# Performance work log

Measured on AMD Instinct MI355X. Metric: run time of the kernel, lower is better.

The kernel has to match this reference:

```python
import jax, jax.numpy as jnp
import numpy as np

B = 4096
D0, D1 = 256, 64


def setup_inputs() -> dict:
    key = jax.random.key(0)
    k0, k1, k2, k3 = jax.random.split(key, 4)
    return {
        "s0": jax.random.normal(k0, (B, D0), dtype=jnp.float32),
        "s1": jax.random.normal(k1, (B, D1), dtype=jnp.float32),
        "t0": jax.random.normal(k2, (B, D0), dtype=jnp.float32),
        "t1": jax.random.normal(k3, (B, D1), dtype=jnp.float32),
    }


def _gaussian_kernel(source, target):
    # feats: [2B, D]
    feats = jnp.concatenate([source, target], axis=0)
    n = feats.shape[0]
    # pairwise squared distances [2B, 2B] via the Gram-matrix identity
    # (same math as ((x - y) ** 2).sum(-1), avoids the [N, N, D] intermediate)
    sq = jnp.sum(feats * feats, axis=-1)
    dist = sq[:, None] + sq[None, :] - 2.0 * (feats @ feats.T)
    # median-heuristic bandwidth with num_kernels=1: gamma = (n^2 - n) / sum(dist)
    gamma = (n * n - n) / jnp.sum(jax.lax.stop_gradient(dist))
    return jnp.exp(-dist * gamma)


def reference(s0, s1, t0, t1):
    # joint kernel: elementwise product of per-stream Gaussian kernels
    k = _gaussian_kernel(s0, t0) * _gaussian_kernel(s1, t1)
    b = s0.shape[0]
    s2s = k[:b, :b]
    t2t = k[b:, b:]
    s2t = k[:b, b:]
    return jnp.mean(s2s + t2t - 2.0 * s2t)
```

## Files before the change

kernel.cpp:

```cpp
#include <hip/hip_runtime.h>
#include <hip/hip_fp8.h>

#define B_ROWS 4096
#define NTOT   8192
#define D0     256
#define D1     64
#define KDIM   320
#define NSB    128
#define NTILE  64
#define NTRI   2080

typedef __attribute__((ext_vector_type(4))) float f32x4;
typedef __attribute__((ext_vector_type(2))) long long2v;

#define OFF_GAM   0
#define OFF_PQ0   32
#define OFF_PQ1   544
#define OFF_P0    1056
#define OFF_P1    132128
#define OFF_R     164896
#define OFF_BSUM  197664
#define OFF_PHI   214304

__device__ __forceinline__ void load_lds16(const void* g, void* l) {
    __builtin_amdgcn_global_load_lds(
        (const __attribute__((address_space(1))) void*)g,
        (__attribute__((address_space(3))) void*)l, 16, 0, 0);
}

#define VMCNT(n) asm volatile("s_waitcnt vmcnt(" #n ")" ::: "memory")
#define BAR()    do { asm volatile("" ::: "memory");            \
                      __builtin_amdgcn_s_barrier();             \
                      asm volatile("" ::: "memory"); } while (0)

__global__ __launch_bounds__(256) void k_stats(
    const float* __restrict__ s0, const float* __restrict__ s1,
    const float* __restrict__ t0, const float* __restrict__ t1,
    float* __restrict__ part0, float* __restrict__ part1,
    float* __restrict__ pq0, float* __restrict__ pq1) {
    __shared__ float sh0[4][256];
    __shared__ float sh1[4][64];
    __shared__ float shq[4][2];
    int t = threadIdx.x, wv = t >> 6, lane = t & 63;
    int rb = blockIdx.x * 64;
    int c4 = lane * 4;
    int rr = wv;

    f32x4 cs = {0.f, 0.f, 0.f, 0.f};
    float q0 = 0.f;
    #pragma unroll 4
    for (int k = 0; k < 16; ++k) {
        int row = rb + rr + k * 4;
        const float* b0 = (row < B_ROWS) ? s0 + (size_t)row * D0 : t0 + (size_t)(row - B_ROWS) * D0;
        f32x4 v = *(const f32x4*)(b0 + c4);
        cs.x += v.x; cs.y += v.y; cs.z += v.z; cs.w += v.w;
        q0 += v.x * v.x + v.y * v.y + v.z * v.z + v.w * v.w;
    }
    *(f32x4*)&sh0[rr][c4] = cs;

    float cs1 = 0.f, q1 = 0.f;
    #pragma unroll 4
    for (int k = 0; k < 16; ++k) {
        int row = rb + rr + k * 4;
        const float* b1 = (row < B_ROWS) ? s1 + (size_t)row * D1 : t1 + (size_t)(row - B_ROWS) * D1;
        float v = b1[lane];
        cs1 += v; q1 += v * v;
    }
    sh1[rr][lane] = cs1;

    #pragma unroll
    for (int o = 32; o; o >>= 1) { q0 += __shfl_xor(q0, o, 64); q1 += __shfl_xor(q1, o, 64); }
    if (lane == 0) { shq[wv][0] = q0; shq[wv][1] = q1; }
    __syncthreads();

    part0[blockIdx.x * D0 + t] = sh0[0][t] + sh0[1][t] + sh0[2][t] + sh0[3][t];
    if (t < D1) part1[blockIdx.x * D1 + t] = sh1[0][t] + sh1[1][t] + sh1[2][t] + sh1[3][t];
    if (t == 0) {
        pq0[blockIdx.x] = shq[0][0] + shq[1][0] + shq[2][0] + shq[3][0];
        pq1[blockIdx.x] = shq[0][1] + shq[1][1] + shq[2][1] + shq[3][1];
    }
}

__global__ __launch_bounds__(256) void k_gamma(
    const float* __restrict__ pq0, const float* __restrict__ pq1,
    const float* __restrict__ part0, const float* __restrict__ part1,
    float* __restrict__ gam) {
    __shared__ double sh[4][4];
    int t = threadIdx.x, wv = t >> 6, lane = t & 63;

    double a0 = 0.0, a1 = 0.0;
    if (t < NSB) { a0 = (double)pq0[t]; a1 = (double)pq1[t]; }

    double F0t = 0.0;
    for (int b = 0; b < NSB; ++b) F0t += (double)part0[b * D0 + t];
    double nf0 = F0t * F0t;

    double nf1 = 0.0;
    if (t < D1) {
        double F1t = 0.0;
        for (int b = 0; b < NSB; ++b) F1t += (double)part1[b * D1 + t];
        nf1 = F1t * F1t;
    }

    #pragma unroll
    for (int o = 32; o; o >>= 1) {
        a0  += __shfl_xor(a0, o, 64);
        a1  += __shfl_xor(a1, o, 64);
        nf0 += __shfl_xor(nf0, o, 64);
        nf1 += __shfl_xor(nf1, o, 64);
    }
    if (lane == 0) { sh[wv][0] = a0; sh[wv][1] = a1; sh[wv][2] = nf0; sh[wv][3] = nf1; }
    __syncthreads();
    if (t == 0) {
        double b0 = 0, b1 = 0, b2 = 0, b3 = 0;
        for (int w = 0; w < 4; ++w) { b0 += sh[w][0]; b1 += sh[w][1]; b2 += sh[w][2]; b3 += sh[w][3]; }
        double n = (double)NTOT;
        double g0 = (n * n - n) / (2.0 * n * b0 - 2.0 * b2);
        double g1 = (n * n - n) / (2.0 * n * b1 - 2.0 * b3);
        gam[0] = (float)g0; gam[1] = (float)g1;
        gam[2] = (float)sqrt(g0); gam[3] = (float)sqrt(g1);
    }
}

__global__ __launch_bounds__(256) void k_pack(
    const float* __restrict__ s0, const float* __restrict__ s1,
    const float* __restrict__ t0, const float* __restrict__ t1,
    const float* __restrict__ gam, unsigned char* __restrict__ phi,
    float* __restrict__ rvec) {
    int wv = threadIdx.x >> 6, lane = threadIdx.x & 63;
    int row = blockIdx.x * 4 + wv;
    float sg0 = gam[2], sg1 = gam[3];
    const float* b0 = (row < B_ROWS) ? s0 + (size_t)row * D0 : t0 + (size_t)(row - B_ROWS) * D0;
    const float* b1 = (row < B_ROWS) ? s1 + (size_t)row * D1 : t1 + (size_t)(row - B_ROWS) * D1;
    unsigned char* pr = phi + (size_t)row * KDIM;
    f32x4 v = *(const f32x4*)(b0 + lane * 4);
    __hip_fp8_e4m3 q0(v.x * sg0), q1(v.y * sg0), q2(v.z * sg0), q3(v.w * sg0);
    unsigned int word = (unsigned int)q0.__x | ((unsigned int)q1.__x << 8) |
                        ((unsigned int)q2.__x << 16) | ((unsigned int)q3.__x << 24);
    int doff0 = ((lane >> 4) << 6) + (((lane >> 1) & 3) << 4) +
                (((lane >> 3) & 1) << 3) + ((lane & 1) << 2);
    *(unsigned int*)(pr + doff0) = word;
    float f0 = (float)q0, f1 = (float)q1, f2 = (float)q2, f3 = (float)q3;
    float p = f0 * f0 + f1 * f1 + f2 * f2 + f3 * f3;
    __hip_fp8_e4m3 qd(b1[lane] * sg1);
    int doff1 = 256 + (((lane >> 3) & 3) << 4) + (((lane >> 5) & 1) << 3) + (lane & 7);
    pr[doff1] = qd.__x;
    float fd = (float)qd;
    p += fd * fd;
    #pragma unroll
    for (int o = 32; o; o >>= 1) p += __shfl_xor(p, o, 64);
    if (lane == 0) rvec[row] = p;
}

__global__ __launch_bounds__(256, 3) void k_mmd(
    const unsigned char* __restrict__ phi, const float* __restrict__ rvec,
    double* __restrict__ blocksum) {
    int tb = blockIdx.x;
    int I = (int)((129.0f - sqrtf(16641.0f - 8.0f * (float)tb)) * 0.5f);
    while ((129 * I - I * I) / 2 > tb) --I;
    while ((129 * (I + 1) - (I + 1) * (I + 1)) / 2 <= tb) ++I;
    int J = I + (tb - (129 * I - I * I) / 2);

    __shared__ unsigned char As[24576];
    __shared__ unsigned char Bs[24576];
    __shared__ float rIl[128], rJl[128];
    __shared__ float wsum[4];

    int tid = threadIdx.x, wv = tid >> 6, lane = tid & 63;
    int wr = wv >> 1, wc = wv & 1;
    int rgrp = lane >> 4, rlow = lane & 15;
    const int rowA = I * 128, rowB = J * 128;

    if (tid < 128) rIl[tid] = rvec[rowA + tid];
    else           rJl[tid - 128] = rvec[rowB + (tid - 128)];
    asm volatile("s_waitcnt lgkmcnt(0)" ::: "memory");

    f32x4 acc_[4][4] = {};

    #define STAGE_CHUNK(c)                                                      \
        _Pragma("unroll")                                                       \
        for (int it = 0; it < 2; ++it) {                                        \
            int idx = it * 256 + tid;                                           \
            int row = idx >> 2, slot = idx & 3;                                 \
            int rg = slot ^ ((row >> 1) & 3);                                   \
            size_t gcol = (size_t)(c) * 64 + rg * 16;                           \
            load_lds16(phi + (size_t)(rowA + row) * KDIM + gcol,                \
                       As + ((c) % 3) * 8192 + it * 4096 + wv * 1024);          \
            load_lds16(phi + (size_t)(rowB + row) * KDIM + gcol,                \
                       Bs + ((c) % 3) * 8192 + it * 4096 + wv * 1024);          \
        }

    #define COMPUTE_SLOT(s)                                                     \
        {                                                                       \
            long2v af[4], bf[4];                                                \
            _Pragma("unroll")                                                   \
            for (int m = 0; m < 4; ++m) {                                       \
                int row = wr * 64 + m * 16 + rlow;                              \
                int sl = rgrp ^ ((row >> 1) & 3);                               \
                af[m] = *(const long2v*)&As[(s) * 8192 + row * 64 + sl * 16];   \
            }                                                                   \
            _Pragma("unroll")                                                   \
            for (int n = 0; n < 4; ++n) {                                       \
                int col = wc * 64 + n * 16 + rlow;                              \
                int sl = rgrp ^ ((col >> 1) & 3);                               \
                bf[n] = *(const long2v*)&Bs[(s) * 8192 + col * 64 + sl * 16];   \
            }                                                                   \
            __builtin_amdgcn_s_setprio(1);                                      \
            _Pragma("unroll")                                                   \
            for (int m = 0; m < 4; ++m)                                         \
                _Pragma("unroll")                                               \
                for (int n = 0; n < 4; ++n) {                                   \
                    acc_[m][n] = __builtin_amdgcn_mfma_f32_16x16x32_fp8_fp8(    \
                        af[m][0], bf[n][0], acc_[m][n], 0, 0, 0);               \
                    acc_[m][n] = __builtin_amdgcn_mfma_f32_16x16x32_fp8_fp8(    \
                        af[m][1], bf[n][1], acc_[m][n], 0, 0, 0);               \
                }                                                               \
            __builtin_amdgcn_s_setprio(0);                                      \
        }

    STAGE_CHUNK(0);
    STAGE_CHUNK(1);
    STAGE_CHUNK(2);

    VMCNT(8); BAR();
    COMPUTE_SLOT(0);
    BAR();
    STAGE_CHUNK(3);
    VMCNT(8); BAR();
    COMPUTE_SLOT(1);
    BAR();
    STAGE_CHUNK(4);
    VMCNT(8); BAR();
    COMPUTE_SLOT(2);
    VMCNT(4); BAR();
    COMPUTE_SLOT(0);
    VMCNT(0); BAR();
    COMPUTE_SLOT(1);

    float psum = 0.f;
    #pragma unroll
    for (int m = 0; m < 4; ++m) {
        float ri[4];
        #pragma unroll
        for (int j = 0; j < 4; ++j) ri[j] = rIl[wr * 64 + m * 16 + rgrp * 4 + j];
        #pragma unroll
        for (int n = 0; n < 4; ++n) {
            float rj = rJl[wc * 64 + n * 16 + rlow];
            f32x4 a = acc_[m][n];
            psum += __expf(2.f * a.x - ri[0] - rj);
            psum += __expf(2.f * a.y - ri[1] - rj);
            psum += __expf(2.f * a.z - ri[2] - rj);
            psum += __expf(2.f * a.w - ri[3] - rj);
        }
    }
    #pragma unroll
    for (int o = 32; o; o >>= 1) psum += __shfl_xor(psum, o, 64);
    if (lane == 0) wsum[wv] = psum;
    __syncthreads();
    if (tid == 0) {
        float bs = wsum[0] + wsum[1] + wsum[2] + wsum[3];
        double sgn = ((I < 32) == (J < 32)) ? 1.0 : -1.0;
        double fac = (I == J) ? 1.0 : 2.0;
        blocksum[tb] = sgn * fac * (double)bs;
    }
}

__global__ __launch_bounds__(256) void k_final(
    const double* __restrict__ blocksum, float* __restrict__ out) {
    __shared__ double sh[4];
    int t = threadIdx.x, wv = t >> 6, lane = t & 63;
    double s = 0.0;
    for (int i = t; i < NTRI; i += 256) s += blocksum[i];
    #pragma unroll
    for (int o = 32; o; o >>= 1) s += __shfl_xor(s, o, 64);
    if (lane == 0) sh[wv] = s;
    __syncthreads();
    if (t == 0) {
        double tot = sh[0] + sh[1] + sh[2] + sh[3];
        out[0] = (float)(tot / ((double)B_ROWS * (double)B_ROWS));
    }
}

extern "C" void kernel_launch(void* const* d_in, const int* in_sizes, int n_in,
                              void* d_out, int out_size, void* d_ws, size_t ws_size,
                              hipStream_t stream) {
    const float* s0 = (const float*)d_in[0];
    const float* s1 = (const float*)d_in[1];
    const float* t0 = (const float*)d_in[2];
    const float* t1 = (const float*)d_in[3];
    char* ws = (char*)d_ws;
    float*  gam  = (float*)(ws + OFF_GAM);
    float*  pq0  = (float*)(ws + OFF_PQ0);
    float*  pq1  = (float*)(ws + OFF_PQ1);
    float*  p0   = (float*)(ws + OFF_P0);
    float*  p1   = (float*)(ws + OFF_P1);
    float*  rvec = (float*)(ws + OFF_R);
    double* bsum = (double*)(ws + OFF_BSUM);
    unsigned char* phi = (unsigned char*)(ws + OFF_PHI);

    k_stats<<<NSB, 256, 0, stream>>>(s0, s1, t0, t1, p0, p1, pq0, pq1);
    k_gamma<<<1, 256, 0, stream>>>(pq0, pq1, p0, p1, gam);
    k_pack<<<2048, 256, 0, stream>>>(s0, s1, t0, t1, gam, phi, rvec);
    k_mmd<<<NTRI, 256, 0, stream>>>(phi, rvec, bsum);
    k_final<<<1, 256, 0, stream>>>(bsum, (float*)d_out);
}
```

Baseline: 51.41 us.

## Shrink MMD Gram tiles to single-wave 64x64 blocks without barriers

The pairwise-kernel kernel now launches one 64-thread wavefront per 64x64 upper-triangular tile (8256 tiles) instead of four waves sharing a 128x128 tile. Because one wave owns its tile, the workgroup barriers go away, the LDS pipeline shrinks to double buffering, and the row norms are read straight from global memory instead of through LDS. This is meant to cut synchronization cost and LDS footprint and to raise occupancy. The trade-off is half the operand reuse per loaded byte, so global/L2 traffic for the phi matrix roughly doubles, and the final reduction has four times as many block sums.

After: 67.75 us. 1.32x slower.

```diff
diff --git a/kernel.cpp b/kernel.cpp
--- a/kernel.cpp
+++ b/kernel.cpp
@@ -7,8 +7,8 @@
 #define D1     64
 #define KDIM   320
 #define NSB    128
-#define NTILE  64
-#define NTRI   2080
+#define NTILE  128
+#define NTRI   8256
 
 typedef __attribute__((ext_vector_type(4))) float f32x4;
 typedef __attribute__((ext_vector_type(2))) long long2v;
@@ -20,7 +20,7 @@
 #define OFF_P1    132128
 #define OFF_R     164896
 #define OFF_BSUM  197664
-#define OFF_PHI   214304
+#define OFF_PHI   263712
 
 __device__ __forceinline__ void load_lds16(const void* g, void* l) {
     __builtin_amdgcn_global_load_lds(
@@ -29,9 +29,7 @@
 }
 
 #define VMCNT(n) asm volatile("s_waitcnt vmcnt(" #n ")" ::: "memory")
-#define BAR()    do { asm volatile("" ::: "memory");            \
-                      __builtin_amdgcn_s_barrier();             \
-                      asm volatile("" ::: "memory"); } while (0)
+#define CFENCE() asm volatile("" ::: "memory")
 
 __global__ __launch_bounds__(256) void k_stats(
     const float* __restrict__ s0, const float* __restrict__ s1,
@@ -152,42 +150,35 @@
     if (lane == 0) rvec[row] = p;
 }
 
-__global__ __launch_bounds__(256, 3) void k_mmd(
+__global__ __launch_bounds__(64) void k_mmd(
     const unsigned char* __restrict__ phi, const float* __restrict__ rvec,
     double* __restrict__ blocksum) {
     int tb = blockIdx.x;
-    int I = (int)((129.0f - sqrtf(16641.0f - 8.0f * (float)tb)) * 0.5f);
-    while ((129 * I - I * I) / 2 > tb) --I;
-    while ((129 * (I + 1) - (I + 1) * (I + 1)) / 2 <= tb) ++I;
-    int J = I + (tb - (129 * I - I * I) / 2);
-
-    __shared__ unsigned char As[24576];
-    __shared__ unsigned char Bs[24576];
-    __shared__ float rIl[128], rJl[128];
-    __shared__ float wsum[4];
-
-    int tid = threadIdx.x, wv = tid >> 6, lane = tid & 63;
-    int wr = wv >> 1, wc = wv & 1;
+    int I = (int)((257.0f - sqrtf(66049.0f - 8.0f * (float)tb)) * 0.5f);
+    while ((257 * I - I * I) / 2 > tb) --I;
+    while ((257 * (I + 1) - (I + 1) * (I + 1)) / 2 <= tb) ++I;
+    int J = I + (tb - (257 * I - I * I) / 2);
+
+    __shared__ unsigned char As[2][4096];
+    __shared__ unsigned char Bs[2][4096];
+
+    int lane = threadIdx.x & 63;
     int rgrp = lane >> 4, rlow = lane & 15;
-    const int rowA = I * 128, rowB = J * 128;
-
-    if (tid < 128) rIl[tid] = rvec[rowA + tid];
-    else           rJl[tid - 128] = rvec[rowB + (tid - 128)];
-    asm volatile("s_waitcnt lgkmcnt(0)" ::: "memory");
+    const int rowA = I * 64, rowB = J * 64;
 
     f32x4 acc_[4][4] = {};
 
     #define STAGE_CHUNK(c)                                                      \
         _Pragma("unroll")                                                       \
-        for (int it = 0; it < 2; ++it) {                                        \
-            int idx = it * 256 + tid;                                           \
-            int row = idx >> 2, slot = idx & 3;                                 \
-            int rg = slot ^ ((row >> 1) & 3);                                   \
+        for (int it = 0; it < 4; ++it) {                                        \
+            int row = it * 16 + (lane >> 2);                                    \
+            int sl = lane & 3;                                                  \
+            int rg = sl ^ ((row >> 1) & 3);                                     \
             size_t gcol = (size_t)(c) * 64 + rg * 16;                           \
             load_lds16(phi + (size_t)(rowA + row) * KDIM + gcol,                \
-                       As + ((c) % 3) * 8192 + it * 4096 + wv * 1024);          \
+                       &As[(c) & 1][it * 1024]);                                \
             load_lds16(phi + (size_t)(rowB + row) * KDIM + gcol,                \
-                       Bs + ((c) % 3) * 8192 + it * 4096 + wv * 1024);          \
+                       &Bs[(c) & 1][it * 1024]);                                \
         }
 
     #define COMPUTE_SLOT(s)                                                     \
@@ -195,15 +186,15 @@
             long2v af[4], bf[4];                                                \
             _Pragma("unroll")                                                   \
             for (int m = 0; m < 4; ++m) {                                       \
-                int row = wr * 64 + m * 16 + rlow;                              \
+                int row = m * 16 + rlow;                                        \
                 int sl = rgrp ^ ((row >> 1) & 3);                               \
-                af[m] = *(const long2v*)&As[(s) * 8192 + row * 64 + sl * 16];   \
+                af[m] = *(const long2v*)&As[(s)][row * 64 + sl * 16];           \
             }                                                                   \
             _Pragma("unroll")                                                   \
             for (int n = 0; n < 4; ++n) {                                       \
-                int col = wc * 64 + n * 16 + rlow;                              \
+                int col = n * 16 + rlow;                                        \
                 int sl = rgrp ^ ((col >> 1) & 3);                               \
-                bf[n] = *(const long2v*)&Bs[(s) * 8192 + col * 64 + sl * 16];   \
+                bf[n] = *(const long2v*)&Bs[(s)][col * 64 + sl * 16];           \
             }                                                                   \
             __builtin_amdgcn_s_setprio(1);                                      \
             _Pragma("unroll")                                                   \
@@ -220,48 +211,33 @@
 
     STAGE_CHUNK(0);
     STAGE_CHUNK(1);
-    STAGE_CHUNK(2);
-
-    VMCNT(8); BAR();
-    COMPUTE_SLOT(0);
-    BAR();
-    STAGE_CHUNK(3);
-    VMCNT(8); BAR();
-    COMPUTE_SLOT(1);
-    BAR();
-    STAGE_CHUNK(4);
-    VMCNT(8); BAR();
-    COMPUTE_SLOT(2);
-    VMCNT(4); BAR();
-    COMPUTE_SLOT(0);
-    VMCNT(0); BAR();
-    COMPUTE_SLOT(1);
+
+    VMCNT(8);  COMPUTE_SLOT(0);  CFENCE();  STAGE_CHUNK(2);
+    VMCNT(8);  COMPUTE_SLOT(1);  CFENCE();  STAGE_CHUNK(3);
+    VMCNT(8);  COMPUTE_SLOT(0);  CFENCE();  STAGE_CHUNK(4);
+    VMCNT(8);  COMPUTE_SLOT(1);
+    VMCNT(0);  COMPUTE_SLOT(0);
 
     float psum = 0.f;
     #pragma unroll
     for (int m = 0; m < 4; ++m) {
-        float ri[4];
-        #pragma unroll
-        for (int j = 0; j < 4; ++j) ri[j] = rIl[wr * 64 + m * 16 + rgrp * 4 + j];
+        f32x4 ri = *(const f32x4*)&rvec[rowA + m * 16 + rgrp * 4];
         #pragma unroll
         for (int n = 0; n < 4; ++n) {
-            float rj = rJl[wc * 64 + n * 16 + rlow];
+            float rj = rvec[rowB + n * 16 + rlow];
             f32x4 a = acc_[m][n];
-            psum += __expf(2.f * a.x - ri[0] - rj);
-            psum += __expf(2.f * a.y - ri[1] - rj);
-            psum += __expf(2.f * a.z - ri[2] - rj);
-            psum += __expf(2.f * a.w - ri[3] - rj);
+            psum += __expf(2.f * a.x - ri.x - rj);
+            psum += __expf(2.f * a.y - ri.y - rj);
+            psum += __expf(2.f * a.z - ri.z - rj);
+            psum += __expf(2.f * a.w - ri.w - rj);
         }
     }
     #pragma unroll
     for (int o = 32; o; o >>= 1) psum += __shfl_xor(psum, o, 64);
-    if (lane == 0) wsum[wv] = psum;
-    __syncthreads();
-    if (tid == 0) {
-        float bs = wsum[0] + wsum[1] + wsum[2] + wsum[3];
-        double sgn = ((I < 32) == (J < 32)) ? 1.0 : -1.0;
+    if (lane == 0) {
+        double sgn = ((I < 64) == (J < 64)) ? 1.0 : -1.0;
         double fac = (I == J) ? 1.0 : 2.0;
-        blocksum[tb] = sgn * fac * (double)bs;
+        blocksum[tb] = sgn * fac * (double)psum;
     }
 }
 
@@ -301,6 +277,6 @@
     k_stats<<<NSB, 256, 0, stream>>>(s0, s1, t0, t1, p0, p1, pq0, pq1);
     k_gamma<<<1, 256, 0, stream>>>(pq0, pq1, p0, p1, gam);
     k_pack<<<2048, 256, 0, stream>>>(s0, s1, t0, t1, gam, phi, rvec);
-    k_mmd<<<NTRI, 256, 0, stream>>>(phi, rvec, bsum);
+    k_mmd<<<NTRI, 64, 0, stream>>>(phi, rvec, bsum);
     k_final<<<1, 256, 0, stream>>>(bsum, (float*)d_out);
 }
```
